# Kernel tuning notes

Measured on AMD Instinct MI355X. Metric: run time of the kernel, lower is better.

## Reference

```python
import jax, jax.numpy as jnp
import numpy as np

EMB = 1024
HEADS = 16
DH = EMB // HEADS
EPS = 1e-5


def _layernorm(x, w, b):
    mean = jnp.mean(x, axis=-1, keepdims=True)
    var = jnp.mean((x - mean) ** 2, axis=-1, keepdims=True)  # unbiased=False
    return w * (x - mean) / jnp.sqrt(var + EPS) + b


def _gelu_tanh(x):
    c = jnp.sqrt(jnp.asarray(2.0 / jnp.pi, x.dtype))
    return 0.5 * x * (1.0 + jnp.tanh(c * (x + 0.044715 * x ** 3)))


def setup_inputs() -> dict:
    key = jax.random.key(0)
    ks = jax.random.split(key, 8)
    B, N = 2, 2048
    s = lambda fan_in: 1.0 / np.sqrt(fan_in)
    # weights stored as [in, out] (torch Linear applied as x @ W.T == x @ W_here)
    return {
        "x": jax.random.normal(ks[0], (B, N, EMB), jnp.float32),
        "ln1_w": jnp.ones((EMB,), jnp.float32),
        "ln1_b": jnp.zeros((EMB,), jnp.float32),
        "w_qkv": jax.random.normal(ks[1], (EMB, 3 * EMB), jnp.float32) * s(EMB),  # qkv_bias=False
        "w_attn_proj": jax.random.normal(ks[2], (EMB, EMB), jnp.float32) * s(EMB),
        "b_attn_proj": jnp.zeros((EMB,), jnp.float32),
        "ln2_w": jnp.ones((EMB,), jnp.float32),
        "ln2_b": jnp.zeros((EMB,), jnp.float32),
        "w_fc": jax.random.normal(ks[3], (EMB, 4 * EMB), jnp.float32) * s(EMB),
        "b_fc": jnp.zeros((4 * EMB,), jnp.float32),
        "w_proj": jax.random.normal(ks[4], (4 * EMB, EMB), jnp.float32) * s(4 * EMB),
        "b_proj": jnp.zeros((EMB,), jnp.float32),
    }


def reference(x, ln1_w, ln1_b, w_qkv, w_attn_proj, b_attn_proj,
              ln2_w, ln2_b, w_fc, b_fc, w_proj, b_proj):
    B, N, _ = x.shape
    # --- attention sublayer (pre-LN) ---
    h = _layernorm(x, ln1_w, ln1_b)
    qkv = h @ w_qkv  # [B,N,3E]
    q, k, v = jnp.split(qkv, 3, axis=-1)
    # [B,H,N,Dh]
    q = q.reshape(B, N, HEADS, DH).transpose(0, 2, 1, 3)
    k = k.reshape(B, N, HEADS, DH).transpose(0, 2, 1, 3)
    v = v.reshape(B, N, HEADS, DH).transpose(0, 2, 1, 3)
    scores = jnp.einsum("bhqd,bhkd->bhqk", q, k) * (DH ** -0.5)
    causal = jnp.tril(jnp.ones((N, N), bool))
    scores = jnp.where(causal, scores, -jnp.inf)
    attn = jax.nn.softmax(scores, axis=-1)  # attn_pdrop=0 (eval)
    ctx = jnp.einsum("bhqk,bhkd->bhqd", attn, v)
    ctx = ctx.transpose(0, 2, 1, 3).reshape(B, N, EMB)
    x = x + (ctx @ w_attn_proj + b_attn_proj)  # resid_pdrop=0
    # --- MLP sublayer (pre-LN) ---
    h = _layernorm(x, ln2_w, ln2_b)
    h = _gelu_tanh(h @ w_fc + b_fc)
    x = x + (h @ w_proj + b_proj)
    return x
```

## Files before the change

kernel.cpp:

```cpp
#include <hip/hip_runtime.h>
#include <stdint.h>

#define EMB 1024
#define NHEAD 16
#define DH 64
#define SEQ 2048
#define NTOK 4096

typedef __attribute__((ext_vector_type(8))) short s16x8;
typedef __attribute__((ext_vector_type(4))) short s16x4;
typedef __attribute__((ext_vector_type(4))) float f32x4;
typedef __attribute__((ext_vector_type(4))) unsigned short u16x4;

__device__ __forceinline__ unsigned short f2bf(float f){
    union { float f; unsigned int u; } v; v.f = f;
    unsigned int r = v.u + 0x7fffu + ((v.u >> 16) & 1u);
    return (unsigned short)(r >> 16);
}

__device__ __forceinline__ f32x4 mfma16(s16x8 a, s16x8 b, f32x4 c){
    return __builtin_amdgcn_mfma_f32_16x16x32_bf16(a, b, c, 0, 0, 0);
}

__device__ __forceinline__ void gload16(const void* g, void* l){
    __builtin_amdgcn_global_load_lds((const __attribute__((address_space(1))) void*)g,
                                     (__attribute__((address_space(3))) void*)l, 16, 0, 0);
}

__device__ __forceinline__ s16x8 cat8(s16x4 a, s16x4 b){
    s16x8 r;
    r[0]=a[0]; r[1]=a[1]; r[2]=a[2]; r[3]=a[3];
    r[4]=b[0]; r[5]=b[1]; r[6]=b[2]; r[7]=b[3];
    return r;
}

__device__ __forceinline__ unsigned cvtpk(float lo, float hi){
    unsigned r;
    asm("v_cvt_pk_bf16_f32 %0, %1, %2" : "=v"(r) : "v"(lo), "v"(hi));
    return r;
}

__device__ __forceinline__ s16x8 qscale(s16x8 q){
    s16x8 r;
    #pragma unroll
    for (int e = 0; e < 8; ++e){
        union { float f; unsigned u; } v;
        v.u = ((unsigned)(unsigned short)q[e]) << 16;
        v.f *= 0.125f;
        r[e] = (short)f2bf(v.f);
    }
    return r;
}

__global__ __launch_bounds__(256) void convT_kernel(const float* __restrict__ in,
                                                    unsigned short* __restrict__ out,
                                                    int R, int C){
    __shared__ float tile[32][33];
    const int c0 = blockIdx.x * 32, r0 = blockIdx.y * 32;
    const int tx = threadIdx.x, ty = threadIdx.y;
    #pragma unroll
    for (int k = 0; k < 4; ++k)
        tile[ty*4+k][tx] = in[(long)(r0 + ty*4 + k) * C + c0 + tx];
    __syncthreads();
    #pragma unroll
    for (int k = 0; k < 4; ++k)
        out[(long)(c0 + ty*4 + k) * R + r0 + tx] = f2bf(tile[tx][ty*4+k]);
}

__global__ __launch_bounds__(256) void vT_kernel(const unsigned short* __restrict__ qkv,
                                                 unsigned short* __restrict__ vtg){
    __shared__ unsigned short tile[64*64];
    const int bh = blockIdx.y, b = bh >> 4, h = bh & 15;
    const int n0 = blockIdx.x * 64;
    const int t = threadIdx.x;
    const int nr = t >> 3, c0 = (t & 7) * 8;
    #pragma unroll
    for (int hh = 0; hh < 2; ++hh){
        const int n = nr + hh*32;
        uint4 vv = *(const uint4*)&qkv[(long)(b*SEQ + n0 + n)*3072 + 2048 + h*64 + c0];
        *(uint4*)((char*)tile + n*128 + ((c0*2) ^ (((n>>3)&7)<<4))) = vv;
    }
    __syncthreads();
    #pragma unroll
    for (int hh = 0; hh < 2; ++hh){
        const int d = nr + hh*32;
        union { unsigned short u[8]; uint4 v; } tmp;
        #pragma unroll
        for (int j = 0; j < 8; ++j){
            const int n = c0 + j;
            tmp.u[j] = *(const unsigned short*)((char*)tile + n*128 + ((d*2) ^ (((n>>3)&7)<<4)));
        }
        *(uint4*)&vtg[((long)bh*64 + d)*2048 + n0 + c0] = tmp.v;
    }
}

__global__ __launch_bounds__(256) void ln_kernel(const float* __restrict__ x,
                                                 const float* __restrict__ w,
                                                 const float* __restrict__ b,
                                                 unsigned short* __restrict__ out){
    const int row = blockIdx.x, tid = threadIdx.x;
    const float4 v = ((const float4*)(x + (long)row * EMB))[tid];
    float s  = v.x + v.y + v.z + v.w;
    float ss = v.x*v.x + v.y*v.y + v.z*v.z + v.w*v.w;
    #pragma unroll
    for (int off = 32; off >= 1; off >>= 1){
        s  += __shfl_xor(s,  off, 64);
        ss += __shfl_xor(ss, off, 64);
    }
    __shared__ float ps[4], pss[4];
    const int wv = tid >> 6;
    if ((tid & 63) == 0){ ps[wv] = s; pss[wv] = ss; }
    __syncthreads();
    s  = ps[0] + ps[1] + ps[2] + ps[3];
    ss = pss[0] + pss[1] + pss[2] + pss[3];
    const float mean = s * (1.0f/EMB);
    const float var  = ss * (1.0f/EMB) - mean*mean;
    const float rstd = rsqrtf(var + 1e-5f);
    const float4 wv4 = ((const float4*)w)[tid];
    const float4 bv4 = ((const float4*)b)[tid];
    u16x4 o;
    o[0] = f2bf((v.x - mean) * rstd * wv4.x + bv4.x);
    o[1] = f2bf((v.y - mean) * rstd * wv4.y + bv4.y);
    o[2] = f2bf((v.z - mean) * rstd * wv4.z + bv4.z);
    o[3] = f2bf((v.w - mean) * rstd * wv4.w + bv4.w);
    *(u16x4*)(out + (long)row * EMB + tid * 4) = o;
}

__global__ __launch_bounds__(256) void red_kernel(const float* __restrict__ p0,
                                                  const float* __restrict__ p1,
                                                  const float* __restrict__ bias,
                                                  const float* __restrict__ resid,
                                                  float* __restrict__ out, int N){
    const long i = ((long)blockIdx.x * 256 + threadIdx.x) * 4;
    const float4 a = *(const float4*)(p0 + i);
    const float4 b = *(const float4*)(p1 + i);
    const float4 r = *(const float4*)(resid + i);
    const float4 bb = *(const float4*)(bias + ((int)i & (N - 1)));
    float4 o;
    o.x = a.x + b.x + r.x + bb.x;
    o.y = a.y + b.y + r.y + bb.y;
    o.z = a.z + b.z + r.z + bb.z;
    o.w = a.w + b.w + r.w + bb.w;
    *(float4*)(out + i) = o;
}

template<int EPI, int SK>
__global__ __launch_bounds__(512, 2) void gemm3_kernel(const unsigned short* __restrict__ A,
                                                       const unsigned short* __restrict__ Bt,
                                                       const float* __restrict__ bias,
                                                       void* __restrict__ out0,
                                                       void* __restrict__ out1,
                                                       int M, int N, int K){
    __shared__ unsigned short As[3][256*64];
    __shared__ unsigned short Bs[3][128*64];
    const int tid = threadIdx.x, lane = tid & 63, w = tid >> 6;
    const int lm = lane & 15, g = lane >> 4;
    const int wr = w >> 1, wc = w & 1;

    const int gx = gridDim.x;
    const int nwg = gx * gridDim.y;
    int id = blockIdx.y * gx + blockIdx.x;
    id = (id & 7) * (nwg >> 3) + (id >> 3);
    const int m0 = (id / gx) * 256, n0 = (id % gx) * 128;
    const int kz = (SK > 1) ? blockIdx.z : 0;
    const int kbase = kz * (K / SK);
    const int NK = (K / SK) / 64;

    const int r8 = tid >> 3;
    const int src = (((tid & 7) * 16) ^ ((r8 & 7) << 4)) >> 1;
    char* AsB = (char*)&As[0][0];
    char* BsB = (char*)&Bs[0][0];

    auto stage = [&](int bu, int kt){
        #pragma unroll
        for (int p = 0; p < 4; ++p)
            gload16(&A[(long)(m0 + p*64 + r8) * K + kt + src], AsB + bu*32768 + p*8192 + tid*16);
        #pragma unroll
        for (int p = 0; p < 2; ++p)
            gload16(&Bt[(long)(n0 + p*64 + r8) * K + kt + src], BsB + bu*16384 + p*8192 + tid*16);
    };

    f32x4 zero = {0.0f, 0.0f, 0.0f, 0.0f};
    f32x4 acc[4][4];
    #pragma unroll
    for (int i = 0; i < 4; ++i)
        #pragma unroll
        for (int j = 0; j < 4; ++j) acc[i][j] = zero;

    stage(0, kbase);
    stage(1, kbase + 64);
    int bk = 0, bs = 2;
    const int axor = (lm & 7) << 4;
    for (int k = 0; k < NK; ++k){
        if (k + 2 < NK) stage(bs, kbase + (k + 2) * 64);
        if (k + 3 <= NK)      asm volatile("s_waitcnt vmcnt(12)" ::: "memory");
        else if (k + 2 <= NK) asm volatile("s_waitcnt vmcnt(6)"  ::: "memory");
        else                  asm volatile("s_waitcnt vmcnt(0)"  ::: "memory");
        __builtin_amdgcn_s_barrier();
        asm volatile("" ::: "memory");
        const char* Ab = AsB + bk*32768;
        const char* Bb = BsB + bk*16384;
        #pragma unroll
        for (int kk = 0; kk < 2; ++kk){
            s16x8 af[4], bf[4];
            #pragma unroll
            for (int i = 0; i < 4; ++i)
                af[i] = *(const s16x8*)(Ab + (wr*64 + i*16 + lm)*128 + ((kk*64 + g*16) ^ axor));
            #pragma unroll
            for (int j = 0; j < 4; ++j)
                bf[j] = *(const s16x8*)(Bb + (wc*64 + j*16 + lm)*128 + ((kk*64 + g*16) ^ axor));
            asm volatile("s_waitcnt lgkmcnt(0)" ::: "memory");
            __builtin_amdgcn_sched_barrier(0);
            __builtin_amdgcn_s_setprio(1);
            #pragma unroll
            for (int i = 0; i < 4; ++i)
                #pragma unroll
                for (int j = 0; j < 4; ++j)
                    acc[i][j] = mfma16(af[i], bf[j], acc[i][j]);
            __builtin_amdgcn_s_setprio(0);
            asm volatile("" ::: "memory");
            __builtin_amdgcn_s_barrier();
            asm volatile("" ::: "memory");
        }
        bk = (bk + 1 == 3) ? 0 : bk + 1;
        bs = (bs + 1 == 3) ? 0 : bs + 1;
    }

    float* po = (SK > 1 && kz == 1) ? (float*)out1 : (float*)out0;
    #pragma unroll
    for (int i = 0; i < 4; ++i){
        #pragma unroll
        for (int r = 0; r < 4; ++r){
            const int row = m0 + wr*64 + i*16 + 4*g + r;
            #pragma unroll
            for (int j = 0; j < 4; ++j){
                const int col = n0 + wc*64 + j*16 + lm;
                const float v = acc[i][j][r];
                if (EPI == 0){
                    ((unsigned short*)out0)[(long)row * N + col] = f2bf(v);
                } else if (EPI == 2){
                    const float xx = v + bias[col];
                    const float z = 0.7978845608f * (xx + 0.044715f * xx * xx * xx);
                    const float gg = xx / (1.0f + __expf(-2.0f * z));
                    ((unsigned short*)out0)[(long)row * N + col] = f2bf(gg);
                } else {
                    po[(long)row * N + col] = v;
                }
            }
        }
    }
}

template<int EPI, int BM, int BN, int WR, int WC, int SK>
__global__ __launch_bounds__(WR*WC*64) void gemm_kernel(const unsigned short* __restrict__ A,
                                                        const unsigned short* __restrict__ Bt,
                                                        const float* __restrict__ bias,
                                                        const float* __restrict__ resid,
                                                        void* __restrict__ out0,
                                                        void* __restrict__ out1,
                                                        int M, int N, int K){
    constexpr int NW = WR * WC;
    constexpr int NT = NW * 64;
    constexpr int FI = BM / (WR * 16);
    constexpr int FJ = BN / (WC * 16);
    __shared__ unsigned short As[2][BM * 32];
    __shared__ unsigned short Bs[2][BN * 32];
    const int tid  = threadIdx.x;
    const int lane = tid & 63, w = tid >> 6;
    const int lm = lane & 15, g = lane >> 4;
    const int wr = w / WC, wc = w % WC;

    const int gx = gridDim.x;
    const int nwg = gx * gridDim.y;
    int id = blockIdx.y * gx + blockIdx.x;
    id = (id & 7) * (nwg >> 3) + (id >> 3);
    const int m0 = (id / gx) * BM, n0 = (id % gx) * BN;
    const int kz = (SK > 1) ? blockIdx.z : 0;
    const int kbase = kz * (K / SK);

    f32x4 zero = {0.0f, 0.0f, 0.0f, 0.0f};
    f32x4 acc[FI][FJ];
    #pragma unroll
    for (int i = 0; i < FI; ++i)
        #pragma unroll
        for (int j = 0; j < FJ; ++j) acc[i][j] = zero;

    auto stage = [&](int kt, int bu){
        #pragma unroll
        for (int p = 0; p < BM/(NT/4); ++p)
            gload16(&A[(long)(m0 + p*(NT/4) + (tid>>2)) * K + kt + (tid&3)*8],
                    (char*)&As[bu][0] + p*(NT*16) + tid*16);
        #pragma unroll
        for (int p = 0; p < BN/(NT/4); ++p)
            gload16(&Bt[(long)(n0 + p*(NT/4) + (tid>>2)) * K + kt + (tid&3)*8],
                    (char*)&Bs[bu][0] + p*(NT*16) + tid*16);
    };

    stage(kbase, 0);
    int cur = 0;
    const int nkt = (K / SK) / 32;
    for (int t = 0; t < nkt; ++t){
        __syncthreads();
        if (t + 1 < nkt) stage(kbase + (t+1)*32, cur ^ 1);
        s16x8 af[FI], bf[FJ];
        #pragma unroll
        for (int i = 0; i < FI; ++i)
            af[i] = *(const s16x8*)&As[cur][(wr*(FI*16) + i*16 + lm)*32 + g*8];
        #pragma unroll
        for (int j = 0; j < FJ; ++j)
            bf[j] = *(const s16x8*)&Bs[cur][(wc*(FJ*16) + j*16 + lm)*32 + g*8];
        #pragma unroll
        for (int i = 0; i < FI; ++i)
            #pragma unroll
            for (int j = 0; j < FJ; ++j)
                acc[i][j] = mfma16(af[i], bf[j], acc[i][j]);
        cur ^= 1;
    }

    float* po = (SK > 1 && kz == 1) ? (float*)out1 : (float*)out0;
    #pragma unroll
    for (int i = 0; i < FI; ++i){
        #pragma unroll
        for (int r = 0; r < 4; ++r){
            const int row = m0 + wr*(FI*16) + i*16 + 4*g + r;
            #pragma unroll
            for (int j = 0; j < FJ; ++j){
                const int col = n0 + wc*(FJ*16) + j*16 + lm;
                const float v = acc[i][j][r];
                if (EPI == 0){
                    ((unsigned short*)out0)[(long)row * N + col] = f2bf(v);
                } else if (EPI == 1){
                    ((float*)out0)[(long)row * N + col] =
                        v + bias[col] + resid[(long)row * N + col];
                } else if (EPI == 2){
                    const float xx = v + bias[col];
                    const float z = 0.7978845608f * (xx + 0.044715f * xx * xx * xx);
                    const float gg = xx / (1.0f + __expf(-2.0f * z));
                    ((unsigned short*)out0)[(long)row * N + col] = f2bf(gg);
                } else {
                    po[(long)row * N + col] = v;
                }
            }
        }
    }
}

__global__ __launch_bounds__(256) void attn_kernel(const unsigned short* __restrict__ qkv,
                                                   const unsigned short* __restrict__ vtg,
                                                   unsigned short* __restrict__ ctx){
    __shared__ unsigned short Ks[2][4096];
    __shared__ unsigned short Vs[2][4096];
    const int pair = blockIdx.x, bh = blockIdx.y;
    const int b = bh >> 4, h = bh & 15;
    const int tid = threadIdx.x, lane = tid & 63, w = tid >> 6;
    const int lm = lane & 15, g = lane >> 4;
    const long qkvb = (long)b * SEQ * 3072;
    const unsigned short* kglob = qkv + qkvb + 1024 + h*64;
    const unsigned short* vglob = vtg + (long)bh * 64 * 2048;

    const int srow = tid >> 3;
    const int soff = (tid & 7) * 16;
    f32x4 zero = {0.0f, 0.0f, 0.0f, 0.0f};

    #pragma unroll 1
    for (int grp = 0; grp < 2; ++grp){
        const int qg = (grp == 0) ? pair : (31 - pair);
        const int q0 = qg * 64;
        const int nt = qg + 1;
        const int qrow = q0 + w*16 + lm;

        const unsigned short* qrp = qkv + qkvb + (long)qrow*3072 + h*64;
        const s16x8 qf0 = qscale(*(const s16x8*)(qrp + g*8));
        const s16x8 qf1 = qscale(*(const s16x8*)(qrp + 32 + g*8));

        f32x4 o[4];
        #pragma unroll
        for (int d = 0; d < 4; ++d) o[d] = zero;
        float mrun = -3e38f, lrun = 0.0f;

        auto stage = [&](int t, int bu){
            const int kv0 = t * 64;
            #pragma unroll
            for (int hh = 0; hh < 2; ++hh){
                const int row = srow + hh*32;
                const int sw  = soff ^ ((row & 7) << 4);
                gload16(kglob + (long)(kv0 + row)*3072 + (sw >> 1),
                        (char*)&Ks[bu][0] + hh*4096 + w*1024);
                gload16(vglob + (long)row*2048 + kv0 + (sw >> 1),
                        (char*)&Vs[bu][0] + hh*4096 + w*1024);
            }
        };

        __syncthreads();
        stage(0, 0);
        int cur = 0;
        #pragma unroll 1
        for (int t = 0; t < nt; ++t){
            __syncthreads();
            if (t + 1 < nt) stage(t + 1, cur ^ 1);

            const char* Kb = (const char*)&Ks[cur][0];
            const int sw = (lm & 7) << 4;
            f32x4 sc[4];
            #pragma unroll
            for (int s = 0; s < 4; ++s){
                const char* rp = Kb + (s*16 + lm)*128;
                s16x8 kf0 = *(const s16x8*)(rp + ((g*16) ^ sw));
                s16x8 kf1 = *(const s16x8*)(rp + ((64 + g*16) ^ sw));
                f32x4 a = mfma16(kf0, qf0, zero);
                sc[s] = mfma16(kf1, qf1, a);
            }

            const bool diag = (t == nt - 1);
            float p[4][4];
            float mx = -3e38f;
            #pragma unroll
            for (int s = 0; s < 4; ++s)
                #pragma unroll
                for (int r = 0; r < 4; ++r){
                    float vv = sc[s][r];
                    if (diag && (s*16 + 4*g + r > w*16 + lm)) vv = -3e38f;
                    p[s][r] = vv;
                    mx = fmaxf(mx, vv);
                }
            mx = fmaxf(mx, __shfl_xor(mx, 16, 64));
            mx = fmaxf(mx, __shfl_xor(mx, 32, 64));
            if (!__all(mx - mrun <= 8.0f)){
                const float mnew = fmaxf(mrun, mx);
                const float corr = __expf(mrun - mnew);
                lrun *= corr;
                #pragma unroll
                for (int d = 0; d < 4; ++d) o[d] *= corr;
                mrun = mnew;
            }
            float rs = 0.0f;
            #pragma unroll
            for (int s = 0; s < 4; ++s)
                #pragma unroll
                for (int r = 0; r < 4; ++r){
                    const float e = __expf(p[s][r] - mrun);
                    p[s][r] = e;
                    rs += e;
                }
            rs += __shfl_xor(rs, 16, 64);
            rs += __shfl_xor(rs, 32, 64);
            lrun += rs;

            union { unsigned u[4]; s16x8 v; } P0, P1;
            P0.u[0] = cvtpk(p[0][0], p[0][1]);
            P0.u[1] = cvtpk(p[0][2], p[0][3]);
            P0.u[2] = cvtpk(p[1][0], p[1][1]);
            P0.u[3] = cvtpk(p[1][2], p[1][3]);
            P1.u[0] = cvtpk(p[2][0], p[2][1]);
            P1.u[1] = cvtpk(p[2][2], p[2][3]);
            P1.u[2] = cvtpk(p[3][0], p[3][1]);
            P1.u[3] = cvtpk(p[3][2], p[3][3]);

            const char* Vb = (const char*)&Vs[cur][0];
            #pragma unroll
            for (int d = 0; d < 4; ++d){
                const char* vrp = Vb + (d*16 + lm)*128;
                s16x4 a0 = *(const s16x4*)(vrp + ((g*8) ^ sw));
                s16x4 a1 = *(const s16x4*)(vrp + ((32 + g*8) ^ sw));
                o[d] = mfma16(cat8(a0, a1), P0.v, o[d]);
                s16x4 b0 = *(const s16x4*)(vrp + ((64 + g*8) ^ sw));
                s16x4 b1 = *(const s16x4*)(vrp + ((96 + g*8) ^ sw));
                o[d] = mfma16(cat8(b0, b1), P1.v, o[d]);
            }
            cur ^= 1;
        }

        const float inv = 1.0f / lrun;
        unsigned short* cw = ctx + (long)(b*SEQ + qrow)*EMB + h*DH + 4*g;
        #pragma unroll
        for (int d = 0; d < 4; ++d){
            u16x4 ov;
            ov[0] = f2bf(o[d][0]*inv); ov[1] = f2bf(o[d][1]*inv);
            ov[2] = f2bf(o[d][2]*inv); ov[3] = f2bf(o[d][3]*inv);
            *(u16x4*)(cw + d*16) = ov;
        }
    }
}

extern "C" void kernel_launch(void* const* d_in, const int* in_sizes, int n_in,
                              void* d_out, int out_size, void* d_ws, size_t ws_size,
                              hipStream_t stream){
    const float* x     = (const float*)d_in[0];
    const float* ln1_w = (const float*)d_in[1];
    const float* ln1_b = (const float*)d_in[2];
    const float* w_qkv = (const float*)d_in[3];
    const float* w_ap  = (const float*)d_in[4];
    const float* b_ap  = (const float*)d_in[5];
    const float* ln2_w = (const float*)d_in[6];
    const float* ln2_b = (const float*)d_in[7];
    const float* w_fc  = (const float*)d_in[8];
    const float* b_fc  = (const float*)d_in[9];
    const float* w_pr  = (const float*)d_in[10];
    const float* b_pr  = (const float*)d_in[11];
    float* out = (float*)d_out;

    char* ws = (char*)d_ws;
    unsigned short* wqkvT = (unsigned short*)(ws + 0);
    unsigned short* wapT  = (unsigned short*)(ws + 6291456);
    unsigned short* wfcT  = (unsigned short*)(ws + 8388608);
    unsigned short* wprT  = (unsigned short*)(ws + 16777216);
    unsigned short* h1    = (unsigned short*)(ws + 25165824);
    unsigned short* vtg   = (unsigned short*)(ws + 25165824);
    unsigned short* qkv   = (unsigned short*)(ws + 33554432);
    unsigned short* ctx   = (unsigned short*)(ws + 58720256);
    float*          x1    = (float*)(ws + 67108864);
    unsigned short* h2    = (unsigned short*)(ws + 83886080);
    unsigned short* afc   = (unsigned short*)(ws + 92274688);
    float* pp0 = (float*)(ws + 0);
    float* pp1 = (float*)(ws + 25165824);

    dim3 b32(32, 8, 1);
    convT_kernel<<<dim3(3072/32, 1024/32), b32, 0, stream>>>(w_qkv, wqkvT, 1024, 3072);
    convT_kernel<<<dim3(1024/32, 1024/32), b32, 0, stream>>>(w_ap,  wapT,  1024, 1024);
    convT_kernel<<<dim3(4096/32, 1024/32), b32, 0, stream>>>(w_fc,  wfcT,  1024, 4096);
    convT_kernel<<<dim3(1024/32, 4096/32), b32, 0, stream>>>(w_pr,  wprT,  4096, 1024);

    ln_kernel<<<NTOK, 256, 0, stream>>>(x, ln1_w, ln1_b, h1);

    gemm3_kernel<0,1><<<dim3(3072/128, NTOK/256), 512, 0, stream>>>(
        h1, wqkvT, nullptr, qkv, nullptr, NTOK, 3072, 1024);

    vT_kernel<<<dim3(SEQ/64, 32), 256, 0, stream>>>(qkv, vtg);

    attn_kernel<<<dim3(16, 32), 256, 0, stream>>>(qkv, vtg, ctx);

    gemm_kernel<1,128,64,2,2,1><<<dim3(1024/64, NTOK/128), 256, 0, stream>>>(
        ctx, wapT, b_ap, x, x1, nullptr, NTOK, 1024, 1024);

    ln_kernel<<<NTOK, 256, 0, stream>>>(x1, ln2_w, ln2_b, h2);

    gemm3_kernel<2,1><<<dim3(4096/128, NTOK/256), 512, 0, stream>>>(
        h2, wfcT, b_fc, afc, nullptr, NTOK, 4096, 1024);

    gemm3_kernel<3,2><<<dim3(1024/128, NTOK/256, 2), 512, 0, stream>>>(
        afc, wprT, nullptr, pp0, pp1, NTOK, 1024, 4096);
    red_kernel<<<NTOK*EMB/1024, 256, 0, stream>>>(pp0, pp1, b_pr, x1, out, EMB);
}
```

Measured before the change: 283.8 us.

## Shrink GEMM tiles to 128x128 double-buffered and software-pipeline attention QK^T

The main GEMM goes from a 512-thread 256x128 tile with a triple-buffered LDS pipeline to a 256-thread 128x128 tile with double buffering and one barrier per k-tile. This doubles the number of workgroups and cuts LDS use, trading operand reuse per tile for occupancy. Separately, the attention kernel moves to a three-stage K/V LDS ring and computes the next tile's QK^T scores before the current tile's softmax and PV, so the score MFMAs overlap with the exponentials. The extra score registers could add register pressure.

```diff
diff --git a/kernel.cpp b/kernel.cpp
--- a/kernel.cpp
+++ b/kernel.cpp
@@ -145,14 +145,14 @@
 }
 
 template<int EPI, int SK>
-__global__ __launch_bounds__(512, 2) void gemm3_kernel(const unsigned short* __restrict__ A,
+__global__ __launch_bounds__(256, 2) void gemm4_kernel(const unsigned short* __restrict__ A,
                                                        const unsigned short* __restrict__ Bt,
                                                        const float* __restrict__ bias,
                                                        void* __restrict__ out0,
                                                        void* __restrict__ out1,
                                                        int M, int N, int K){
-    __shared__ unsigned short As[3][256*64];
-    __shared__ unsigned short Bs[3][128*64];
+    __shared__ unsigned short As[2][128*64];
+    __shared__ unsigned short Bs[2][128*64];
     const int tid = threadIdx.x, lane = tid & 63, w = tid >> 6;
     const int lm = lane & 15, g = lane >> 4;
     const int wr = w >> 1, wc = w & 1;
@@ -161,10 +161,10 @@
     const int nwg = gx * gridDim.y;
     int id = blockIdx.y * gx + blockIdx.x;
     id = (id & 7) * (nwg >> 3) + (id >> 3);
-    const int m0 = (id / gx) * 256, n0 = (id % gx) * 128;
+    const int m0 = (id / gx) * 128, n0 = (id % gx) * 128;
     const int kz = (SK > 1) ? blockIdx.z : 0;
     const int kbase = kz * (K / SK);
-    const int NK = (K / SK) / 64;
+    const int nkt = (K / SK) / 64;
 
     const int r8 = tid >> 3;
     const int src = (((tid & 7) * 16) ^ ((r8 & 7) << 4)) >> 1;
@@ -174,10 +174,10 @@
     auto stage = [&](int bu, int kt){
         #pragma unroll
         for (int p = 0; p < 4; ++p)
-            gload16(&A[(long)(m0 + p*64 + r8) * K + kt + src], AsB + bu*32768 + p*8192 + tid*16);
-        #pragma unroll
-        for (int p = 0; p < 2; ++p)
-            gload16(&Bt[(long)(n0 + p*64 + r8) * K + kt + src], BsB + bu*16384 + p*8192 + tid*16);
+            gload16(&A[(long)(m0 + p*32 + r8) * K + kt + src], AsB + bu*16384 + p*4096 + tid*16);
+        #pragma unroll
+        for (int p = 0; p < 4; ++p)
+            gload16(&Bt[(long)(n0 + p*32 + r8) * K + kt + src], BsB + bu*16384 + p*4096 + tid*16);
     };
 
     f32x4 zero = {0.0f, 0.0f, 0.0f, 0.0f};
@@ -188,18 +188,19 @@
         for (int j = 0; j < 4; ++j) acc[i][j] = zero;
 
     stage(0, kbase);
-    stage(1, kbase + 64);
-    int bk = 0, bs = 2;
+    int cur = 0;
     const int axor = (lm & 7) << 4;
-    for (int k = 0; k < NK; ++k){
-        if (k + 2 < NK) stage(bs, kbase + (k + 2) * 64);
-        if (k + 3 <= NK)      asm volatile("s_waitcnt vmcnt(12)" ::: "memory");
-        else if (k + 2 <= NK) asm volatile("s_waitcnt vmcnt(6)"  ::: "memory");
-        else                  asm volatile("s_waitcnt vmcnt(0)"  ::: "memory");
+    for (int t = 0; t < nkt; ++t){
+        if (t + 1 < nkt){
+            stage(cur ^ 1, kbase + (t + 1) * 64);
+            asm volatile("s_waitcnt vmcnt(8)" ::: "memory");
+        } else {
+            asm volatile("s_waitcnt vmcnt(0)" ::: "memory");
+        }
         __builtin_amdgcn_s_barrier();
         asm volatile("" ::: "memory");
-        const char* Ab = AsB + bk*32768;
-        const char* Bb = BsB + bk*16384;
+        const char* Ab = AsB + cur*16384;
+        const char* Bb = BsB + cur*16384;
         #pragma unroll
         for (int kk = 0; kk < 2; ++kk){
             s16x8 af[4], bf[4];
@@ -218,12 +219,11 @@
                 for (int j = 0; j < 4; ++j)
                     acc[i][j] = mfma16(af[i], bf[j], acc[i][j]);
             __builtin_amdgcn_s_setprio(0);
-            asm volatile("" ::: "memory");
-            __builtin_amdgcn_s_barrier();
-            asm volatile("" ::: "memory");
-        }
-        bk = (bk + 1 == 3) ? 0 : bk + 1;
-        bs = (bs + 1 == 3) ? 0 : bs + 1;
+        }
+        asm volatile("" ::: "memory");
+        __builtin_amdgcn_s_barrier();
+        asm volatile("" ::: "memory");
+        cur ^= 1;
     }
 
     float* po = (SK > 1 && kz == 1) ? (float*)out1 : (float*)out0;
@@ -348,8 +348,8 @@
 __global__ __launch_bounds__(256) void attn_kernel(const unsigned short* __restrict__ qkv,
                                                    const unsigned short* __restrict__ vtg,
                                                    unsigned short* __restrict__ ctx){
-    __shared__ unsigned short Ks[2][4096];
-    __shared__ unsigned short Vs[2][4096];
+    __shared__ unsigned short Ks[3][4096];
+    __shared__ unsigned short Vs[3][4096];
     const int pair = blockIdx.x, bh = blockIdx.y;
     const int b = bh >> 4, h = bh & 15;
     const int tid = threadIdx.x, lane = tid & 63, w = tid >> 6;
@@ -360,6 +360,7 @@
 
     const int srow = tid >> 3;
     const int soff = (tid & 7) * 16;
+    const int swz = (lm & 7) << 4;
     f32x4 zero = {0.0f, 0.0f, 0.0f, 0.0f};
 
     #pragma unroll 1
@@ -378,7 +379,7 @@
         for (int d = 0; d < 4; ++d) o[d] = zero;
         float mrun = -3e38f, lrun = 0.0f;
 
-        auto stage = [&](int t, int bu){
+        auto stageKV = [&](int t, int bu){
             const int kv0 = t * 64;
             #pragma unroll
             for (int hh = 0; hh < 2; ++hh){
@@ -390,25 +391,42 @@
                         (char*)&Vs[bu][0] + hh*4096 + w*1024);
             }
         };
-
-        __syncthreads();
-        stage(0, 0);
-        int cur = 0;
+        auto qkt = [&](int bu, f32x4* sc){
+            const char* Kb = (const char*)&Ks[bu][0];
+            #pragma unroll
+            for (int s = 0; s < 4; ++s){
+                const char* rp = Kb + (s*16 + lm)*128;
+                s16x8 kf0 = *(const s16x8*)(rp + ((g*16) ^ swz));
+                s16x8 kf1 = *(const s16x8*)(rp + ((64 + g*16) ^ swz));
+                f32x4 a = mfma16(kf0, qf0, zero);
+                sc[s] = mfma16(kf1, qf1, a);
+            }
+        };
+
+        __builtin_amdgcn_s_barrier();
+        asm volatile("" ::: "memory");
+        stageKV(0, 0);
+        if (nt > 1){
+            stageKV(1, 1);
+            asm volatile("s_waitcnt vmcnt(4)" ::: "memory");
+        } else {
+            asm volatile("s_waitcnt vmcnt(0)" ::: "memory");
+        }
+        __builtin_amdgcn_s_barrier();
+        asm volatile("" ::: "memory");
+
+        f32x4 sc[4], scN[4];
+        qkt(0, sc);
+
         #pragma unroll 1
         for (int t = 0; t < nt; ++t){
-            __syncthreads();
-            if (t + 1 < nt) stage(t + 1, cur ^ 1);
-
-            const char* Kb = (const char*)&Ks[cur][0];
-            const int sw = (lm & 7) << 4;
-            f32x4 sc[4];
-            #pragma unroll
-            for (int s = 0; s < 4; ++s){
-                const char* rp = Kb + (s*16 + lm)*128;
-                s16x8 kf0 = *(const s16x8*)(rp + ((g*16) ^ sw));
-                s16x8 kf1 = *(const s16x8*)(rp + ((64 + g*16) ^ sw));
-                f32x4 a = mfma16(kf0, qf0, zero);
-                sc[s] = mfma16(kf1, qf1, a);
+            const bool more = (t + 1 < nt);
+            if (more){
+                asm volatile("s_waitcnt vmcnt(0)" ::: "memory");
+                __builtin_amdgcn_s_barrier();
+                asm volatile("" ::: "memory");
+                if (t + 2 < nt) stageKV(t + 2, (t + 2) % 3);
+                qkt((t + 1) % 3, scN);
             }
 
             const bool diag = (t == nt - 1);
@@ -456,18 +474,21 @@
             P1.u[2] = cvtpk(p[3][0], p[3][1]);
             P1.u[3] = cvtpk(p[3][2], p[3][3]);
 
-            const char* Vb = (const char*)&Vs[cur][0];
+            const char* Vb = (const char*)&Vs[t % 3][0];
             #pragma unroll
             for (int d = 0; d < 4; ++d){
                 const char* vrp = Vb + (d*16 + lm)*128;
-                s16x4 a0 = *(const s16x4*)(vrp + ((g*8) ^ sw));
-                s16x4 a1 = *(const s16x4*)(vrp + ((32 + g*8) ^ sw));
+                s16x4 a0 = *(const s16x4*)(vrp + ((g*8) ^ swz));
+                s16x4 a1 = *(const s16x4*)(vrp + ((32 + g*8) ^ swz));
                 o[d] = mfma16(cat8(a0, a1), P0.v, o[d]);
-                s16x4 b0 = *(const s16x4*)(vrp + ((64 + g*8) ^ sw));
-                s16x4 b1 = *(const s16x4*)(vrp + ((96 + g*8) ^ sw));
+                s16x4 b0 = *(const s16x4*)(vrp + ((64 + g*8) ^ swz));
+                s16x4 b1 = *(const s16x4*)(vrp + ((96 + g*8) ^ swz));
                 o[d] = mfma16(cat8(b0, b1), P1.v, o[d]);
             }
-            cur ^= 1;
+            if (more){
+                #pragma unroll
+                for (int s4 = 0; s4 < 4; ++s4) sc[s4] = scN[s4];
+            }
         }
 
         const float inv = 1.0f / lrun;
@@ -522,7 +543,7 @@
 
     ln_kernel<<<NTOK, 256, 0, stream>>>(x, ln1_w, ln1_b, h1);
 
-    gemm3_kernel<0,1><<<dim3(3072/128, NTOK/256), 512, 0, stream>>>(
+    gemm4_kernel<0,1><<<dim3(3072/128, NTOK/128), 256, 0, stream>>>(
         h1, wqkvT, nullptr, qkv, nullptr, NTOK, 3072, 1024);
 
     vT_kernel<<<dim3(SEQ/64, 32), 256, 0, stream>>>(qkv, vtg);
@@ -534,10 +555,10 @@
 
     ln_kernel<<<NTOK, 256, 0, stream>>>(x1, ln2_w, ln2_b, h2);
 
-    gemm3_kernel<2,1><<<dim3(4096/128, NTOK/256), 512, 0, stream>>>(
+    gemm4_kernel<2,1><<<dim3(4096/128, NTOK/128), 256, 0, stream>>>(
         h2, wfcT, b_fc, afc, nullptr, NTOK, 4096, 1024);
 
-    gemm3_kernel<3,2><<<dim3(1024/128, NTOK/256, 2), 512, 0, stream>>>(
+    gemm4_kernel<3,2><<<dim3(1024/128, NTOK/128, 2), 256, 0, stream>>>(
         afc, wprT, nullptr, pp0, pp1, NTOK, 1024, 4096);
     red_kernel<<<NTOK*EMB/1024, 256, 0, stream>>>(pp0, pp1, b_pr, x1, out, EMB);
 }
```

New measurement: 253.1 us. 10.8% less time.
